# Kernel optimization log

Measured on AMD Instinct MI355X. Metric: run time of the kernel, lower is better.

Reference implementation:

```python
import jax, jax.numpy as jnp
import numpy as np

N, F_IN, F_OUT = 200000, 128, 64
H, DEG = 50000, 32            # num_hyperedges, nodes per hyperedge
E = H * DEG                   # total incidences


def setup_inputs() -> dict:
    key = jax.random.key(0)
    k1, k2, k3, k4 = jax.random.split(key, 4)
    x = jax.random.normal(k1, (N, F_IN), dtype=jnp.float32)
    W = jax.random.normal(k2, (F_OUT, F_IN), dtype=jnp.float32) / np.sqrt(F_IN)
    a = jax.random.normal(k3, (2 * F_OUT,), dtype=jnp.float32) / np.sqrt(2 * F_OUT)
    nodes = jax.random.randint(k4, (E,), 0, N, dtype=jnp.int32)
    edges = jnp.repeat(jnp.arange(H, dtype=jnp.int32), DEG)  # sorted edge ids, DEG nodes each
    hyperedge_index = jnp.stack([nodes, edges])  # (2, E)
    return {"x": x, "W": W, "a": a, "hyperedge_index": hyperedge_index}


def reference(x, W, a, hyperedge_index):
    # h = W x  (Linear without bias, weight stored as (out, in))
    h = x @ W.T                                   # (N, F_OUT)
    nodes = hyperedge_index[0]
    eid = hyperedge_index[1]                      # sorted, groups incidences per hyperedge

    # attention score for ordered pair (j,k): a[:F] . h_j + a[F:] . h_k
    s1 = h @ a[:F_OUT]                            # (N,) left-slot contribution per node
    s2 = h @ a[F_OUT:]                            # (N,) right-slot contribution per node
    s1e = s1[nodes]                               # (E,)
    s2e = s2[nodes]                               # (E,)

    counts = jax.ops.segment_sum(jnp.ones_like(eid), eid, num_segments=H)   # degree per edge
    starts = jnp.cumsum(counts) - counts
    rank = jnp.arange(E, dtype=eid.dtype) - starts[eid]                     # position within edge
    deg_e = counts[eid]
    # sum over pairs j<k of (s1_j + s2_k):
    #   node at rank r appears (deg-1-r) times in left slot, r times in right slot
    w1 = (deg_e - 1 - rank).astype(h.dtype)
    w2 = rank.astype(h.dtype)
    pair_sum = jax.ops.segment_sum(s1e * w1 + s2e * w2, eid, num_segments=H)
    npairs = (counts * (counts - 1)) // 2
    edge_attention = pair_sum / jnp.maximum(npairs, 1).astype(h.dtype)      # mean over pairs
    # all H edges have DEG>=2 nodes by construction, matching torch's non-empty filter
    return h, edge_attention
```

## Files before the change

### kernel.cpp

```cpp
#include <hip/hip_runtime.h>

#define F_IN  128
#define F_OUT 64
#define DEG   32

typedef __attribute__((ext_vector_type(8))) short  short8;
typedef __attribute__((ext_vector_type(4))) float  float4v;

__device__ __forceinline__ unsigned short f2bf(float f) {
    unsigned int u = __builtin_bit_cast(unsigned int, f);
    u += 0x7FFFu + ((u >> 16) & 1u);
    return (unsigned short)(u >> 16);
}

__device__ __forceinline__ short8 cvt8(float4v lo, float4v hi) {
    short8 r;
    r[0] = (short)f2bf(lo[0]); r[1] = (short)f2bf(lo[1]);
    r[2] = (short)f2bf(lo[2]); r[3] = (short)f2bf(lo[3]);
    r[4] = (short)f2bf(hi[0]); r[5] = (short)f2bf(hi[1]);
    r[6] = (short)f2bf(hi[2]); r[7] = (short)f2bf(hi[3]);
    return r;
}

__device__ __forceinline__ short8 load_cvt8(const float* __restrict__ p) {
    const float4v* q = (const float4v*)p;
    return cvt8(q[0], q[1]);
}

__global__ __launch_bounds__(256) void gemm_s12_kernel(
    const float* __restrict__ x, const float* __restrict__ W,
    const float* __restrict__ a, float* __restrict__ h_out,
    float2* __restrict__ s12, int N)
{
    __shared__ short8 wfrag[1024];

    const int tid = threadIdx.x;

#pragma unroll
    for (int i0 = 0; i0 < 1024; i0 += 256) {
        const int i     = i0 + tid;
        const int combo = i >> 6;
        const int sl    = i & 63;
        const int t  = combo >> 2;
        const int ks = combo & 3;
        const int n  = (sl & 15) + 16 * t;
        const int qq = sl >> 4;
        wfrag[i] = load_cvt8(W + n * F_IN + ks * 32 + qq * 8);
    }
    __syncthreads();

    const int lane = tid & 63;
    const int wave = tid >> 6;
    const int row_base = (blockIdx.x * 4 + wave) * 32;
    if (row_base >= N) return;

    const int m = lane & 15;
    const int q = lane >> 4;

    float a1v[4], a2v[4];
#pragma unroll
    for (int t = 0; t < 4; ++t) {
        a1v[t] = a[m + 16 * t];
        a2v[t] = a[F_OUT + m + 16 * t];
    }

#pragma unroll
    for (int s = 0; s < 2; ++s) {
        const int row0 = row_base + s * 16;
        const float* rowp = x + (size_t)(row0 + m) * F_IN + q * 8;

        float4v raw[4][2];
#pragma unroll
        for (int ks = 0; ks < 4; ++ks) {
            const float4v* p = (const float4v*)(rowp + ks * 32);
            raw[ks][0] = p[0];
            raw[ks][1] = p[1];
        }
        short8 afrag[4];
#pragma unroll
        for (int ks = 0; ks < 4; ++ks) afrag[ks] = cvt8(raw[ks][0], raw[ks][1]);

        float4v acc[4];
#pragma unroll
        for (int t = 0; t < 4; ++t) acc[t] = (float4v){0.f, 0.f, 0.f, 0.f};

#pragma unroll
        for (int ks = 0; ks < 4; ++ks) {
#pragma unroll
            for (int t = 0; t < 4; ++t) {
                acc[t] = __builtin_amdgcn_mfma_f32_16x16x32_bf16(
                            afrag[ks], wfrag[(t * 4 + ks) * 64 + lane], acc[t], 0, 0, 0);
            }
        }

        const int rrow = row0 + q * 4;
        float p1[4] = {0.f, 0.f, 0.f, 0.f};
        float p2[4] = {0.f, 0.f, 0.f, 0.f};
#pragma unroll
        for (int t = 0; t < 4; ++t) {
            const int col = m + 16 * t;
#pragma unroll
            for (int r = 0; r < 4; ++r) {
                const float v = acc[t][r];
                h_out[(size_t)(rrow + r) * F_OUT + col] = v;
                p1[r] += v * a1v[t];
                p2[r] += v * a2v[t];
            }
        }
#pragma unroll
        for (int d = 1; d < 16; d <<= 1) {
#pragma unroll
            for (int r = 0; r < 4; ++r) {
                p1[r] += __shfl_xor(p1[r], d);
                p2[r] += __shfl_xor(p2[r], d);
            }
        }
        if (m == 0) {
#pragma unroll
            for (int r = 0; r < 4; ++r)
                s12[rrow + r] = make_float2(p1[r], p2[r]);
        }
    }
}

__global__ __launch_bounds__(256) void edge_att_kernel(
    const int* __restrict__ nodes, const float2* __restrict__ s12,
    float* __restrict__ eatt, int H)
{
    const int t = blockIdx.x * 256 + threadIdx.x;
    const int e = t >> 5;
    const int r = t & 31;
    if (e >= H) return;
    const int node = nodes[(size_t)e * DEG + r];
    const float2 s = s12[node];
    float v = s.x * (float)(DEG - 1 - r) + s.y * (float)r;
#pragma unroll
    for (int d = 1; d < 32; d <<= 1) v += __shfl_xor(v, d);
    if (r == 0) eatt[e] = v * (1.0f / 496.0f);
}

extern "C" void kernel_launch(void* const* d_in, const int* in_sizes, int n_in,
                              void* d_out, int out_size, void* d_ws, size_t ws_size,
                              hipStream_t stream)
{
    const float* x   = (const float*)d_in[0];
    const float* W   = (const float*)d_in[1];
    const float* a   = (const float*)d_in[2];
    const int*   hei = (const int*)d_in[3];

    const int N = in_sizes[0] / F_IN;
    const int E = in_sizes[3] / 2;
    const int H = E / DEG;
    const int* nodes = hei;

    float*  h_out = (float*)d_out;
    float*  eatt  = (float*)d_out + (size_t)N * F_OUT;
    float2* s12   = (float2*)d_ws;

    const int waves  = (N + 31) / 32;
    const int blocks = (waves + 3) / 4;
    gemm_s12_kernel<<<blocks, 256, 0, stream>>>(x, W, a, h_out, s12, N);

    const int eblocks = (E + 255) / 256;
    edge_att_kernel<<<eblocks, 256, 0, stream>>>(nodes, s12, eatt, H);
}
```

Baseline: 190.6 us.

## Make GEMM kernel persistent with double-buffered row loads and packed bf16 conversion

```diff
diff --git a/kernel.cpp b/kernel.cpp
--- a/kernel.cpp
+++ b/kernel.cpp
@@ -1,4 +1,5 @@
 #include <hip/hip_runtime.h>
+#include <hip/hip_bf16.h>
 
 #define F_IN  128
 #define F_OUT 64
@@ -7,18 +8,20 @@
 typedef __attribute__((ext_vector_type(8))) short  short8;
 typedef __attribute__((ext_vector_type(4))) float  float4v;
 
-__device__ __forceinline__ unsigned short f2bf(float f) {
-    unsigned int u = __builtin_bit_cast(unsigned int, f);
-    u += 0x7FFFu + ((u >> 16) & 1u);
-    return (unsigned short)(u >> 16);
+__device__ __forceinline__ short2 pk2(float a, float b) {
+    __hip_bfloat162_raw pr = __float22bfloat162_rn(make_float2(a, b));
+    short2 r;
+    r.x = (short)pr.x;
+    r.y = (short)pr.y;
+    return r;
 }
 
 __device__ __forceinline__ short8 cvt8(float4v lo, float4v hi) {
+    short2 p0 = pk2(lo[0], lo[1]), p1 = pk2(lo[2], lo[3]);
+    short2 p2 = pk2(hi[0], hi[1]), p3 = pk2(hi[2], hi[3]);
     short8 r;
-    r[0] = (short)f2bf(lo[0]); r[1] = (short)f2bf(lo[1]);
-    r[2] = (short)f2bf(lo[2]); r[3] = (short)f2bf(lo[3]);
-    r[4] = (short)f2bf(hi[0]); r[5] = (short)f2bf(hi[1]);
-    r[6] = (short)f2bf(hi[2]); r[7] = (short)f2bf(hi[3]);
+    r[0] = p0.x; r[1] = p0.y; r[2] = p1.x; r[3] = p1.y;
+    r[4] = p2.x; r[5] = p2.y; r[6] = p3.x; r[7] = p3.y;
     return r;
 }
 
@@ -27,7 +30,16 @@
     return cvt8(q[0], q[1]);
 }
 
-__global__ __launch_bounds__(256) void gemm_s12_kernel(
+__device__ __forceinline__ void load8(float4v* dst, const float* __restrict__ p) {
+#pragma unroll
+    for (int ks = 0; ks < 4; ++ks) {
+        const float4v* pv = (const float4v*)(p + ks * 32);
+        dst[2 * ks]     = pv[0];
+        dst[2 * ks + 1] = pv[1];
+    }
+}
+
+__global__ __launch_bounds__(256, 4) void gemm_s12_kernel(
     const float* __restrict__ x, const float* __restrict__ W,
     const float* __restrict__ a, float* __restrict__ h_out,
     float2* __restrict__ s12, int N)
@@ -51,11 +63,12 @@
 
     const int lane = tid & 63;
     const int wave = tid >> 6;
-    const int row_base = (blockIdx.x * 4 + wave) * 32;
-    if (row_base >= N) return;
-
     const int m = lane & 15;
     const int q = lane >> 4;
+
+    const int wglobal = blockIdx.x * 4 + wave;
+    const int stride  = gridDim.x * 4;
+    const int nstrip  = N >> 4;
 
     float a1v[4], a2v[4];
 #pragma unroll
@@ -64,36 +77,31 @@
         a2v[t] = a[F_OUT + m + 16 * t];
     }
 
-#pragma unroll
-    for (int s = 0; s < 2; ++s) {
-        const int row0 = row_base + s * 16;
-        const float* rowp = x + (size_t)(row0 + m) * F_IN + q * 8;
+    const float* lanebase = x + (size_t)m * F_IN + q * 8;
 
-        float4v raw[4][2];
-#pragma unroll
-        for (int ks = 0; ks < 4; ++ks) {
-            const float4v* p = (const float4v*)(rowp + ks * 32);
-            raw[ks][0] = p[0];
-            raw[ks][1] = p[1];
-        }
+    float4v rawA[8], rawB[8];
+    int s = wglobal;
+    if (s >= nstrip) return;
+    load8(rawA, lanebase + (size_t)s * 16 * F_IN);
+
+    auto compute = [&](const float4v* raw, int sIdx) {
         short8 afrag[4];
 #pragma unroll
-        for (int ks = 0; ks < 4; ++ks) afrag[ks] = cvt8(raw[ks][0], raw[ks][1]);
+        for (int ks = 0; ks < 4; ++ks)
+            afrag[ks] = cvt8(raw[2 * ks], raw[2 * ks + 1]);
 
         float4v acc[4];
 #pragma unroll
         for (int t = 0; t < 4; ++t) acc[t] = (float4v){0.f, 0.f, 0.f, 0.f};
-
 #pragma unroll
         for (int ks = 0; ks < 4; ++ks) {
 #pragma unroll
-            for (int t = 0; t < 4; ++t) {
+            for (int t = 0; t < 4; ++t)
                 acc[t] = __builtin_amdgcn_mfma_f32_16x16x32_bf16(
                             afrag[ks], wfrag[(t * 4 + ks) * 64 + lane], acc[t], 0, 0, 0);
-            }
         }
 
-        const int rrow = row0 + q * 4;
+        const int rrow = sIdx * 16 + q * 4;
         float p1[4] = {0.f, 0.f, 0.f, 0.f};
         float p2[4] = {0.f, 0.f, 0.f, 0.f};
 #pragma unroll
@@ -120,6 +128,19 @@
             for (int r = 0; r < 4; ++r)
                 s12[rrow + r] = make_float2(p1[r], p2[r]);
         }
+    };
+
+    while (true) {
+        int s2 = s + stride;
+        if (s2 < nstrip) load8(rawB, lanebase + (size_t)s2 * 16 * F_IN);
+        compute(rawA, s);
+        if (s2 >= nstrip) break;
+        s = s2;
+        int s3 = s + stride;
+        if (s3 < nstrip) load8(rawA, lanebase + (size_t)s3 * 16 * F_IN);
+        compute(rawB, s);
+        if (s3 >= nstrip) break;
+        s = s3;
     }
 }
 
@@ -157,9 +178,7 @@
     float*  eatt  = (float*)d_out + (size_t)N * F_OUT;
     float2* s12   = (float2*)d_ws;
 
-    const int waves  = (N + 31) / 32;
-    const int blocks = (waves + 3) / 4;
-    gemm_s12_kernel<<<blocks, 256, 0, stream>>>(x, W, a, h_out, s12, N);
+    gemm_s12_kernel<<<1024, 256, 0, stream>>>(x, W, a, h_out, s12, N);
 
     const int eblocks = (E + 255) / 256;
     edge_att_kernel<<<eblocks, 256, 0, stream>>>(nodes, s12, eatt, H);
```

Result: slower. 211.0 us (+10.7%).
